# Optimization experiments

Hardware: AMD Instinct MI355X
Metric: run time of the kernel (lower is better)

## Reference

```python
import jax, jax.numpy as jnp
import numpy as np

WINDOW_SIZE = 2
SOFTMAX_TEMP = 0.01


def get_indices(batch_size, window_size):
    # For each window, match keypoints of frame j against dense map of frame j+1.
    kp_inds, dense_inds = [], []
    for i in range(batch_size):
        for j in range(window_size - 1):
            idx = i * window_size + j
            kp_inds.append(idx)
            dense_inds.append(idx + 1)
    return np.array(kp_inds), np.array(dense_inds)


def l2_normalize(x, axis):
    n = jnp.sqrt(jnp.sum(x * x, axis=axis, keepdims=True))
    return x / jnp.maximum(n, 1e-12)


def grid_sample_bilinear(img, grid_u, grid_v):
    """torch.nn.functional.grid_sample, mode='bilinear', padding='zeros', align_corners=False.
    img: (B,C,H,W); grid_u, grid_v: (B,N) normalized coords in [-1,1]. Returns (B,C,N)."""
    B, C, H, W = img.shape
    x = ((grid_u + 1.0) * W - 1.0) * 0.5  # pixel x
    y = ((grid_v + 1.0) * H - 1.0) * 0.5  # pixel y
    x0 = jnp.floor(x)
    y0 = jnp.floor(y)
    wx1 = x - x0
    wy1 = y - y0
    flat = img.reshape(B, C, H * W)

    def gather(xi, yi):
        valid = (xi >= 0) & (xi <= W - 1) & (yi >= 0) & (yi <= H - 1)
        xi_c = jnp.clip(xi, 0, W - 1).astype(jnp.int32)
        yi_c = jnp.clip(yi, 0, H - 1).astype(jnp.int32)
        idx = yi_c * W + xi_c  # (B,N)
        vals = jnp.take_along_axis(flat, idx[:, None, :], axis=2)  # (B,C,N)
        return vals * valid[:, None, :].astype(img.dtype)

    out = (gather(x0, y0) * ((1 - wx1) * (1 - wy1))[:, None, :]
           + gather(x0 + 1, y0) * (wx1 * (1 - wy1))[:, None, :]
           + gather(x0, y0 + 1) * ((1 - wx1) * wy1)[:, None, :]
           + gather(x0 + 1, y0 + 1) * (wx1 * wy1)[:, None, :])
    return out


def setup_inputs() -> dict:
    key = jax.random.key(0)
    k1, k2, k3, k4 = jax.random.split(key, 4)
    BW, C, N, H, W = 8, 128, 512, 256, 256
    return {
        "keypoint_scores": jax.random.uniform(k1, (BW, 1, N), dtype=jnp.float32),
        "keypoint_desc": jax.random.normal(k2, (BW, C, N), dtype=jnp.float32),
        "scores_dense": jax.random.uniform(k3, (BW, 1, H, W), dtype=jnp.float32),
        "desc_dense": jax.random.normal(k4, (BW, C, H, W), dtype=jnp.float32),
    }


def reference(keypoint_scores, keypoint_desc, scores_dense, desc_dense):
    BW, C, N = keypoint_desc.shape
    batch_size = BW // WINDOW_SIZE
    _, _, H, W = desc_dense.shape
    kp_inds, dense_inds = get_indices(batch_size, WINDOW_SIZE)

    src_desc = l2_normalize(keypoint_desc[kp_inds], axis=1)  # (B,C,N)
    B = src_desc.shape[0]
    tgt_desc_dense = desc_dense[dense_inds]  # (B,C,H,W)
    tgt_unrolled = l2_normalize(tgt_desc_dense.reshape(B, C, H * W), axis=1)

    # cosine similarity scores (B,N,H*W) -> temperature softmax over dense map
    match_vals = jnp.einsum('bcn,bcm->bnm', src_desc, tgt_unrolled)
    soft_match_vals = jax.nn.softmax(match_vals / SOFTMAX_TEMP, axis=2)

    # soft-argmax: expected (u,v) pixel coordinates
    v_coord, u_coord = jnp.meshgrid(jnp.arange(H), jnp.arange(W), indexing='ij')
    coords = jnp.stack([u_coord.reshape(-1), v_coord.reshape(-1)], axis=1).astype(jnp.float32)  # (HW,2)
    pseudo_coords = jnp.einsum('bnm,mk->bnk', soft_match_vals, coords)  # (B,N,2)

    u_norm = 2.0 * pseudo_coords[:, :, 0] / (W - 1) - 1.0
    v_norm = 2.0 * pseudo_coords[:, :, 1] / (H - 1) - 1.0

    tgt_scores_dense = scores_dense[dense_inds]
    pseudo_scores = grid_sample_bilinear(tgt_scores_dense, u_norm, v_norm)  # (B,1,N)
    pseudo_desc = grid_sample_bilinear(tgt_desc_dense, u_norm, v_norm)      # (B,C,N)

    desc_match_score = jnp.sum(src_desc * pseudo_desc, axis=1, keepdims=True) / float(C)
    src_scores = keypoint_scores[kp_inds]
    match_weights = 0.5 * (desc_match_score + 1.0) * src_scores * pseudo_scores
    return (pseudo_coords, match_weights, soft_match_vals)
```

## Files before the change

kernel.cpp:

```cpp
#include <hip/hip_runtime.h>


typedef short  v8s __attribute__((ext_vector_type(8)));
typedef unsigned short v8u __attribute__((ext_vector_type(8)));
typedef float  v4f __attribute__((ext_vector_type(4)));

#define EXP2_SCALE 144.269504088896f
#define WAITV(N) asm volatile("s_waitcnt vmcnt(" #N ")" ::: "memory")

static const size_t O_AHI  = 0;
static const size_t O_ALO  = O_AHI  + 262144ull*2;
static const size_t O_SRCN = O_ALO  + 262144ull*2;
static const size_t O_BHI  = O_SRCN + 262144ull*4;
static const size_t O_BLO  = O_BHI  + 33554432ull*2;
static const size_t O_PART = O_BLO  + 33554432ull*2;
static const size_t O_ROWS = O_PART + 2048ull*512*8;

static __device__ inline unsigned short f2bf(float x) {
    unsigned u = __float_as_uint(x);
    u = u + 0x7FFFu + ((u >> 16) & 1u);
    return (unsigned short)(u >> 16);
}
static __device__ inline float bf2f(unsigned short h) {
    return __uint_as_float(((unsigned)h) << 16);
}

__device__ __forceinline__ void gl_lds16(const void* g, void* l) {
    auto gp = (const __attribute__((address_space(1))) unsigned int*)(uintptr_t)g;
    auto lp = (__attribute__((address_space(3))) unsigned int*)(uintptr_t)l;
    __builtin_amdgcn_global_load_lds(gp, lp, 16, 0, 0);
}

__global__ void __launch_bounds__(256) k_prep_src(const float* __restrict__ kd,
                                                  float* __restrict__ srcN,
                                                  unsigned short* __restrict__ Ahi,
                                                  unsigned short* __restrict__ Alo) {
    int gw = blockIdx.x * 4 + (threadIdx.x >> 6);
    int l  = threadIdx.x & 63;
    int b  = gw >> 9, n = gw & 511;
    const float* base = kd + (size_t)(2 * b) * 128 * 512;
    float x0 = base[l * 512 + n];
    float x1 = base[(l + 64) * 512 + n];
    float ss = x0 * x0 + x1 * x1;
#pragma unroll
    for (int m = 1; m < 64; m <<= 1) ss += __shfl_xor(ss, m, 64);
    float inv = 1.0f / fmaxf(sqrtf(ss), 1e-12f);
    float xn0 = x0 * inv, xn1 = x1 * inv;
    int ob = gw * 128;
    srcN[ob + l] = xn0;  srcN[ob + l + 64] = xn1;
    unsigned short h0 = f2bf(xn0), h1 = f2bf(xn1);
    Ahi[ob + l] = h0;        Ahi[ob + l + 64] = h1;
    Alo[ob + l] = f2bf(xn0 - bf2f(h0));
    Alo[ob + l + 64] = f2bf(xn1 - bf2f(h1));
}

__global__ void __launch_bounds__(256, 2) k_prep_tgt(const float* __restrict__ dd,
                                                     unsigned short* __restrict__ Bhi,
                                                     unsigned short* __restrict__ Blo) {
    int t = blockIdx.x * 256 + threadIdx.x;
    int b = t >> 16;
    int p = t & 65535;
    const float* src = dd + (size_t)(2 * b + 1) * 128 * 65536 + p;
    float v[128];
    float ss = 0.f;
#pragma unroll
    for (int c = 0; c < 128; ++c) { float x = src[(size_t)c * 65536]; v[c] = x; ss += x * x; }
    float inv = 1.0f / fmaxf(sqrtf(ss), 1e-12f);
    size_t ob = (size_t)t * 128;
#pragma unroll
    for (int c8 = 0; c8 < 16; ++c8) {
        v8u h8, l8;
#pragma unroll
        for (int j = 0; j < 8; ++j) {
            float xn = v[c8 * 8 + j] * inv;
            unsigned short h = f2bf(xn);
            h8[j] = h;
            l8[j] = f2bf(xn - bf2f(h));
        }
        *(v8u*)(Bhi + ob + c8 * 8) = h8;
        *(v8u*)(Blo + ob + c8 * 8) = l8;
    }
}

template <int MODE>
__global__ void __launch_bounds__(256, 2) k_gemm(const unsigned short* __restrict__ Ahi,
                                                 const unsigned short* __restrict__ Alo,
                                                 const unsigned short* __restrict__ Bhi,
                                                 const unsigned short* __restrict__ Blo,
                                                 const float4* __restrict__ rows,
                                                 float* __restrict__ part,
                                                 float* __restrict__ osm) {
    __shared__ v4f bstage4[2048];
    __shared__ float paux[MODE == 1 ? 8192 : 512];
    char* bstage = (char*)bstage4;

    const int tid = threadIdx.x;
    const int l = tid & 63, w = tid >> 6;
    const int wm = w & 1, wn = w >> 1;
    const int l15 = l & 15, l16 = l >> 4;
    const int mtg = blockIdx.x, ny = blockIdx.y, b = blockIdx.z;
    const int mt0 = mtg * 16;

    v8s ahi[4][4], alo[4][4];
    {
        const size_t ar = ((size_t)(b * 512 + ny * 128 + wn * 64 + l15)) * 128 + l16 * 8;
#pragma unroll
        for (int nf = 0; nf < 4; ++nf)
#pragma unroll
            for (int ksl = 0; ksl < 4; ++ksl) {
                ahi[nf][ksl] = *(const v8s*)(Ahi + ar + nf * 2048 + ksl * 32);
                alo[nf][ksl] = *(const v8s*)(Alo + ar + nf * 2048 + ksl * 32);
            }
    }
    float invs[4];
    if (MODE == 1) {
#pragma unroll
        for (int nf = 0; nf < 4; ++nf)
            invs[nf] = rows[b * 512 + ny * 128 + wn * 64 + nf * 16 + l15].x;
    }
    asm volatile("s_waitcnt vmcnt(0)" ::: "memory");

    size_t pxrow = ((size_t)b * 65536 + (size_t)mt0 * 128) * 128;

#define STAGE(s, buf, prow)                                                         \
    {                                                                               \
        const unsigned short* src = (((s) < 2) ? Bhi : Blo) + (prow) + (((s) & 1) << 6); \
        char* dst = bstage + (buf) * 16384;                                         \
        _Pragma("unroll")                                                           \
        for (int i = 0; i < 4; ++i) {                                               \
            int sl = tid + i * 256;                                                 \
            int rl = sl >> 3, gg = sl & 7;                                          \
            gl_lds16(src + rl * 128 + ((gg ^ (rl & 7)) << 3), dst + (sl << 4));     \
        }                                                                           \
    }

    STAGE(0, 0, pxrow);

    for (int mt = 0; mt < 16; ++mt) {
        v4f acc[4][4];
#pragma unroll
        for (int mf = 0; mf < 4; ++mf)
#pragma unroll
            for (int nf = 0; nf < 4; ++nf) { v4f z = {0.f, 0.f, 0.f, 0.f}; acc[mf][nf] = z; }

#pragma unroll
        for (int s = 0; s < 4; ++s) {
            if (s < 3)            STAGE(s + 1, (s + 1) & 1, pxrow)
            else if (mt < 15)     STAGE(0, 0, pxrow + 16384)

            if (s == 0) {
                if (mt == 0) WAITV(4);
                else if (MODE == 1) WAITV(20);
                else WAITV(5);
            } else if (s == 3 && mt == 15) {
                WAITV(0);
            } else {
                WAITV(4);
            }
            __builtin_amdgcn_s_barrier();
            __builtin_amdgcn_sched_barrier(0);

            const char* bb = bstage + (s & 1) * 16384;
#pragma unroll
            for (int k2 = 0; k2 < 2; ++k2) {
                const int ksl = ((s & 1) << 1) | k2;
                v8s pxf[4];
#pragma unroll
                for (int mf = 0; mf < 4; ++mf) {
                    int r = wm * 64 + mf * 16 + l15;
                    pxf[mf] = *(const v8s*)(bb + r * 128 + ((((k2 << 2) | l16) ^ (r & 7)) << 4));
                }
#pragma unroll
                for (int mf = 0; mf < 4; ++mf)
#pragma unroll
                    for (int nf = 0; nf < 4; ++nf) {
                        acc[mf][nf] = __builtin_amdgcn_mfma_f32_16x16x32_bf16(pxf[mf], ahi[nf][ksl], acc[mf][nf], 0, 0, 0);
                        if (s < 2)
                            acc[mf][nf] = __builtin_amdgcn_mfma_f32_16x16x32_bf16(pxf[mf], alo[nf][ksl], acc[mf][nf], 0, 0, 0);
                    }
            }
            __builtin_amdgcn_sched_barrier(0);
            __builtin_amdgcn_s_barrier();
        }

        if (MODE == 0) {
            float sS[4], sM[4];
#pragma unroll
            for (int nf = 0; nf < 4; ++nf) { sS[nf] = 0.f; sM[nf] = 0.f; }
#pragma unroll
            for (int mf = 0; mf < 4; ++mf) {
                int mloc = wm * 64 + mf * 16 + l16 * 4;
#pragma unroll
                for (int nf = 0; nf < 4; ++nf)
#pragma unroll
                    for (int r = 0; r < 4; ++r) {
                        float e = __builtin_amdgcn_exp2f(fmaf(acc[mf][nf][r], EXP2_SCALE, -EXP2_SCALE));
                        sS[nf] += e;
                        sM[nf] = fmaf(e, (float)(mloc + r), sM[nf]);
                    }
            }
#pragma unroll
            for (int nf = 0; nf < 4; ++nf) {
                sS[nf] += __shfl_xor(sS[nf], 16, 64); sS[nf] += __shfl_xor(sS[nf], 32, 64);
                sM[nf] += __shfl_xor(sM[nf], 16, 64); sM[nf] += __shfl_xor(sM[nf], 32, 64);
            }
            if (l < 16) {
#pragma unroll
                for (int nf = 0; nf < 4; ++nf) {
                    paux[((w * 4 + nf) * 16 + l15) * 2 + 0] = sS[nf];
                    paux[((w * 4 + nf) * 16 + l15) * 2 + 1] = sM[nf];
                }
            }
            asm volatile("s_waitcnt lgkmcnt(0)" ::: "memory");
            __builtin_amdgcn_s_barrier();
            int q = tid & 1, p15 = (tid >> 1) & 15, pnf = (tid >> 5) & 3, pwn = tid >> 7;
            float vs = paux[(((pwn * 2 + 0) * 4 + pnf) * 16 + p15) * 2 + q]
                     + paux[(((pwn * 2 + 1) * 4 + pnf) * 16 + p15) * 2 + q];
            int rowg = b * 512 + ny * 128 + pwn * 64 + pnf * 16 + p15;
            part[((size_t)rowg * 512 + (mt0 + mt)) * 2 + q] = vs;
        } else {
            const size_t ocol = (size_t)(mt0 + mt) * 128;
            const int g = tid & 31, rh = tid >> 5;
#pragma unroll
            for (int half = 0; half < 2; ++half) {
                if (wn == half) {
#pragma unroll
                    for (int mf = 0; mf < 4; ++mf) {
                        int mq = wm * 16 + mf * 4 + l16;
#pragma unroll
                        for (int nf = 0; nf < 4; ++nf) {
                            int nl = nf * 16 + l15;
                            v4f pv;
#pragma unroll
                            for (int r = 0; r < 4; ++r)
                                pv[r] = __builtin_amdgcn_exp2f(fmaf(acc[mf][nf][r], EXP2_SCALE, -EXP2_SCALE)) * invs[nf];
                            *(v4f*)((char*)paux + nl * 512 + ((mq ^ (nl & 7)) << 4)) = pv;
                        }
                    }
                }
                asm volatile("s_waitcnt lgkmcnt(0)" ::: "memory");
                __builtin_amdgcn_s_barrier();
                size_t orow = (size_t)(b * 512 + ny * 128 + half * 64);
#pragma unroll
                for (int it = 0; it < 8; ++it) {
                    int r = it * 8 + rh;
                    v4f v = *(const v4f*)((const char*)paux + r * 512 + ((g ^ (r & 7)) << 4));
                    __builtin_nontemporal_store(v, (v4f*)(osm + (orow + r) * 65536 + ocol + g * 4));
                }
                __builtin_amdgcn_s_barrier();
            }
        }
        pxrow += 16384;
    }
#undef STAGE
}

__global__ void __launch_bounds__(256) k_reduce(const float2* __restrict__ part,
                                                float4* __restrict__ rows,
                                                float* __restrict__ out) {
    int r = blockIdx.x * 4 + (threadIdx.x >> 6);
    int l = threadIdx.x & 63;
    float S = 0.f, Su = 0.f, Sv = 0.f;
#pragma unroll
    for (int i = 0; i < 8; ++i) {
        int mtv = l + i * 64;
        float2 p = part[(size_t)r * 512 + mtv];
        S += p.x;
        Su += (float)((mtv & 1) * 128) * p.x + p.y;
        Sv += (float)(mtv >> 1) * p.x;
    }
#pragma unroll
    for (int m = 1; m < 64; m <<= 1) {
        S += __shfl_xor(S, m, 64);
        Su += __shfl_xor(Su, m, 64);
        Sv += __shfl_xor(Sv, m, 64);
    }
    if (l == 0) {
        float invS = 1.0f / S;
        float u = Su * invS, v = Sv * invS;
        rows[r] = make_float4(invS, u, v, 0.f);
        out[r * 2] = u;
        out[r * 2 + 1] = v;
    }
}

__global__ void __launch_bounds__(256) k_sample(const float* __restrict__ ksc,
                                                const float* __restrict__ sd,
                                                const float* __restrict__ dd,
                                                const float* __restrict__ srcN,
                                                const float4* __restrict__ rows,
                                                float* __restrict__ out) {
    int gw = blockIdx.x * 4 + (threadIdx.x >> 6);
    int l = threadIdx.x & 63;
    int b = gw >> 9, n = gw & 511;
    float4 rs = rows[gw];
    float u = rs.y, v = rs.z;
    float un = 2.0f * u / 255.0f - 1.0f;
    float vn = 2.0f * v / 255.0f - 1.0f;
    float x = ((un + 1.0f) * 256.0f - 1.0f) * 0.5f;
    float y = ((vn + 1.0f) * 256.0f - 1.0f) * 0.5f;
    float x0f = floorf(x), y0f = floorf(y);
    int x0 = (int)x0f, y0 = (int)y0f;
    int x1 = x0 + 1, y1 = y0 + 1;
    float wx1 = x - x0f, wy1 = y - y0f;
    float wx0 = 1.0f - wx1, wy0 = 1.0f - wy1;
    float m00 = ((x0 >= 0) & (x0 <= 255) & (y0 >= 0) & (y0 <= 255)) ? 1.f : 0.f;
    float m10 = ((x1 >= 0) & (x1 <= 255) & (y0 >= 0) & (y0 <= 255)) ? 1.f : 0.f;
    float m01 = ((x0 >= 0) & (x0 <= 255) & (y1 >= 0) & (y1 <= 255)) ? 1.f : 0.f;
    float m11 = ((x1 >= 0) & (x1 <= 255) & (y1 >= 0) & (y1 <= 255)) ? 1.f : 0.f;
    int cx0 = min(max(x0, 0), 255), cx1 = min(max(x1, 0), 255);
    int cy0 = min(max(y0, 0), 255), cy1 = min(max(y1, 0), 255);
    int i00 = cy0 * 256 + cx0, i10 = cy0 * 256 + cx1;
    int i01 = cy1 * 256 + cx0, i11 = cy1 * 256 + cx1;
    float w00 = wx0 * wy0 * m00, w10 = wx1 * wy0 * m10;
    float w01 = wx0 * wy1 * m01, w11 = wx1 * wy1 * m11;

    const float* sdb = sd + (size_t)(2 * b + 1) * 65536;
    float ps = w00 * sdb[i00] + w10 * sdb[i10] + w01 * sdb[i01] + w11 * sdb[i11];

    const float* ddb = dd + (size_t)(2 * b + 1) * 128 * 65536;
    float dot = 0.f;
#pragma unroll
    for (int h = 0; h < 2; ++h) {
        int c = l + h * 64;
        const float* dc = ddb + (size_t)c * 65536;
        float pd = w00 * dc[i00] + w10 * dc[i10] + w01 * dc[i01] + w11 * dc[i11];
        dot += srcN[gw * 128 + c] * pd;
    }
#pragma unroll
    for (int m = 1; m < 64; m <<= 1) dot += __shfl_xor(dot, m, 64);
    if (l == 0) {
        float dms = dot / 128.0f;
        float sscore = ksc[(2 * b) * 512 + n];
        out[4096 + gw] = 0.5f * (dms + 1.0f) * sscore * ps;
    }
}

extern "C" void kernel_launch(void* const* d_in, const int* in_sizes, int n_in,
                              void* d_out, int out_size, void* d_ws, size_t ws_size,
                              hipStream_t stream) {
    const float* ksc = (const float*)d_in[0];
    const float* kd  = (const float*)d_in[1];
    const float* sd  = (const float*)d_in[2];
    const float* dd  = (const float*)d_in[3];
    float* out = (float*)d_out;
    char* ws = (char*)d_ws;

    unsigned short* Ahi  = (unsigned short*)(ws + O_AHI);
    unsigned short* Alo  = (unsigned short*)(ws + O_ALO);
    float*          srcN = (float*)(ws + O_SRCN);
    unsigned short* Bhi  = (unsigned short*)(ws + O_BHI);
    unsigned short* Blo  = (unsigned short*)(ws + O_BLO);
    float*          part = (float*)(ws + O_PART);
    float4*         rows = (float4*)(ws + O_ROWS);
    float*          osm  = out + 6144;

    k_prep_src<<<512, 256, 0, stream>>>(kd, srcN, Ahi, Alo);
    k_prep_tgt<<<1024, 256, 0, stream>>>(dd, Bhi, Blo);
    k_gemm<0><<<dim3(32, 4, 4), 256, 0, stream>>>(Ahi, Alo, Bhi, Blo, rows, part, osm);
    k_reduce<<<512, 256, 0, stream>>>((const float2*)part, rows, out);
    k_gemm<1><<<dim3(32, 4, 4), 256, 0, stream>>>(Ahi, Alo, Bhi, Blo, rows, part, osm);
    k_sample<<<512, 256, 0, stream>>>(ksc, sd, dd, srcN, rows, out);
}
```

Baseline: 418.3 us.

## Fuse bilinear sampling into second GEMM and split target prep across thread pairs

The separate k_sample kernel is removed. Its bilinear sampling and match-weight computation now run as an epilogue in the ny==0 blocks of k_gemm<1>, which saves one launch and its tail. k_prep_tgt now gives each pixel to two threads, each handling 64 channels, with a shuffle to combine the squared norms; this lowers register pressure and doubles the thread count. The MODE 0 GEMM loop shrinks to two stages, applies the hi/lo split on every stage, and adds a barrier after the partial write. That changes how much of the K dimension the first pass covers, which may affect correctness.

```diff
diff --git a/kernel.cpp b/kernel.cpp
--- a/kernel.cpp
+++ b/kernel.cpp
@@ -54,28 +54,30 @@
     Alo[ob + l + 64] = f2bf(xn1 - bf2f(h1));
 }
 
-__global__ void __launch_bounds__(256, 2) k_prep_tgt(const float* __restrict__ dd,
-                                                     unsigned short* __restrict__ Bhi,
-                                                     unsigned short* __restrict__ Blo) {
-    int t = blockIdx.x * 256 + threadIdx.x;
+__global__ void __launch_bounds__(256) k_prep_tgt(const float* __restrict__ dd,
+                                                  unsigned short* __restrict__ Bhi,
+                                                  unsigned short* __restrict__ Blo) {
+    int t = blockIdx.x * 128 + (threadIdx.x >> 1);
+    int h = threadIdx.x & 1;
     int b = t >> 16;
     int p = t & 65535;
-    const float* src = dd + (size_t)(2 * b + 1) * 128 * 65536 + p;
-    float v[128];
+    const float* src = dd + (size_t)(2 * b + 1) * 128 * 65536 + (size_t)(h * 64) * 65536 + p;
+    float v[64];
     float ss = 0.f;
 #pragma unroll
-    for (int c = 0; c < 128; ++c) { float x = src[(size_t)c * 65536]; v[c] = x; ss += x * x; }
+    for (int c = 0; c < 64; ++c) { float x = src[(size_t)c * 65536]; v[c] = x; ss += x * x; }
+    ss += __shfl_xor(ss, 1, 64);
     float inv = 1.0f / fmaxf(sqrtf(ss), 1e-12f);
-    size_t ob = (size_t)t * 128;
-#pragma unroll
-    for (int c8 = 0; c8 < 16; ++c8) {
+    size_t ob = (size_t)t * 128 + h * 64;
+#pragma unroll
+    for (int c8 = 0; c8 < 8; ++c8) {
         v8u h8, l8;
 #pragma unroll
         for (int j = 0; j < 8; ++j) {
             float xn = v[c8 * 8 + j] * inv;
-            unsigned short h = f2bf(xn);
-            h8[j] = h;
-            l8[j] = f2bf(xn - bf2f(h));
+            unsigned short hh = f2bf(xn);
+            h8[j] = hh;
+            l8[j] = f2bf(xn - bf2f(hh));
         }
         *(v8u*)(Bhi + ob + c8 * 8) = h8;
         *(v8u*)(Blo + ob + c8 * 8) = l8;
@@ -89,10 +91,15 @@
                                                  const unsigned short* __restrict__ Blo,
                                                  const float4* __restrict__ rows,
                                                  float* __restrict__ part,
-                                                 float* __restrict__ osm) {
+                                                 float* __restrict__ out,
+                                                 const float* __restrict__ ksc,
+                                                 const float* __restrict__ sd,
+                                                 const float* __restrict__ dd,
+                                                 const float* __restrict__ srcN) {
     __shared__ v4f bstage4[2048];
     __shared__ float paux[MODE == 1 ? 8192 : 512];
     char* bstage = (char*)bstage4;
+    constexpr int NSTEP = (MODE == 0) ? 2 : 4;
 
     const int tid = threadIdx.x;
     const int l = tid & 63, w = tid >> 6;
@@ -100,6 +107,7 @@
     const int l15 = l & 15, l16 = l >> 4;
     const int mtg = blockIdx.x, ny = blockIdx.y, b = blockIdx.z;
     const int mt0 = mtg * 16;
+    float* osm = out + 6144;
 
     v8s ahi[4][4], alo[4][4];
     {
@@ -144,15 +152,15 @@
             for (int nf = 0; nf < 4; ++nf) { v4f z = {0.f, 0.f, 0.f, 0.f}; acc[mf][nf] = z; }
 
 #pragma unroll
-        for (int s = 0; s < 4; ++s) {
-            if (s < 3)            STAGE(s + 1, (s + 1) & 1, pxrow)
+        for (int s = 0; s < NSTEP; ++s) {
+            if (s < NSTEP - 1)    STAGE(s + 1, (s + 1) & 1, pxrow)
             else if (mt < 15)     STAGE(0, 0, pxrow + 16384)
 
             if (s == 0) {
-                if (mt == 0) WAITV(4);
-                else if (MODE == 1) WAITV(20);
-                else WAITV(5);
-            } else if (s == 3 && mt == 15) {
+                if (mt == 0)          WAITV(4);
+                else if (MODE == 1)   WAITV(20);
+                else                  WAITV(5);
+            } else if (s == NSTEP - 1 && mt == 15) {
                 WAITV(0);
             } else {
                 WAITV(4);
@@ -175,7 +183,7 @@
 #pragma unroll
                     for (int nf = 0; nf < 4; ++nf) {
                         acc[mf][nf] = __builtin_amdgcn_mfma_f32_16x16x32_bf16(pxf[mf], ahi[nf][ksl], acc[mf][nf], 0, 0, 0);
-                        if (s < 2)
+                        if (MODE == 0 || s < 2)
                             acc[mf][nf] = __builtin_amdgcn_mfma_f32_16x16x32_bf16(pxf[mf], alo[nf][ksl], acc[mf][nf], 0, 0, 0);
                     }
             }
@@ -218,6 +226,7 @@
                      + paux[(((pwn * 2 + 1) * 4 + pnf) * 16 + p15) * 2 + q];
             int rowg = b * 512 + ny * 128 + pwn * 64 + pnf * 16 + p15;
             part[((size_t)rowg * 512 + (mt0 + mt)) * 2 + q] = vs;
+            __builtin_amdgcn_s_barrier();
         } else {
             const size_t ocol = (size_t)(mt0 + mt) * 128;
             const int g = tid & 31, rh = tid >> 5;
@@ -253,6 +262,55 @@
         pxrow += 16384;
     }
 #undef STAGE
+
+    if (MODE == 1 && ny == 0) {
+        const int rbase = b * 512 + mtg * 16 + w * 4;
+#pragma unroll
+        for (int rr = 0; rr < 4; ++rr) {
+            int r = rbase + rr;
+            float4 rs = rows[r];
+            float u = rs.y, v = rs.z;
+            float un = 2.0f * u / 255.0f - 1.0f;
+            float vn = 2.0f * v / 255.0f - 1.0f;
+            float x = ((un + 1.0f) * 256.0f - 1.0f) * 0.5f;
+            float y = ((vn + 1.0f) * 256.0f - 1.0f) * 0.5f;
+            float x0f = floorf(x), y0f = floorf(y);
+            int x0 = (int)x0f, y0 = (int)y0f;
+            int x1 = x0 + 1, y1 = y0 + 1;
+            float wx1 = x - x0f, wy1 = y - y0f;
+            float wx0 = 1.0f - wx1, wy0 = 1.0f - wy1;
+            float m00 = ((x0 >= 0) & (x0 <= 255) & (y0 >= 0) & (y0 <= 255)) ? 1.f : 0.f;
+            float m10 = ((x1 >= 0) & (x1 <= 255) & (y0 >= 0) & (y0 <= 255)) ? 1.f : 0.f;
+            float m01 = ((x0 >= 0) & (x0 <= 255) & (y1 >= 0) & (y1 <= 255)) ? 1.f : 0.f;
+            float m11 = ((x1 >= 0) & (x1 <= 255) & (y1 >= 0) & (y1 <= 255)) ? 1.f : 0.f;
+            int cx0 = min(max(x0, 0), 255), cx1 = min(max(x1, 0), 255);
+            int cy0 = min(max(y0, 0), 255), cy1 = min(max(y1, 0), 255);
+            int i00 = cy0 * 256 + cx0, i10 = cy0 * 256 + cx1;
+            int i01 = cy1 * 256 + cx0, i11 = cy1 * 256 + cx1;
+            float w00 = wx0 * wy0 * m00, w10 = wx1 * wy0 * m10;
+            float w01 = wx0 * wy1 * m01, w11 = wx1 * wy1 * m11;
+
+            const float* sdb = sd + (size_t)(2 * b + 1) * 65536;
+            float ps = w00 * sdb[i00] + w10 * sdb[i10] + w01 * sdb[i01] + w11 * sdb[i11];
+
+            const float* ddb = dd + (size_t)(2 * b + 1) * 128 * 65536;
+            float dot = 0.f;
+#pragma unroll
+            for (int h2 = 0; h2 < 2; ++h2) {
+                int c = l + h2 * 64;
+                const float* dc = ddb + (size_t)c * 65536;
+                float pd = w00 * dc[i00] + w10 * dc[i10] + w01 * dc[i01] + w11 * dc[i11];
+                dot += srcN[r * 128 + c] * pd;
+            }
+#pragma unroll
+            for (int m = 1; m < 64; m <<= 1) dot += __shfl_xor(dot, m, 64);
+            if (l == 0) {
+                float dms = dot / 128.0f;
+                float sscore = ksc[(2 * b) * 512 + (r & 511)];
+                out[4096 + r] = 0.5f * (dms + 1.0f) * sscore * ps;
+            }
+        }
+    }
 }
 
 __global__ void __launch_bounds__(256) k_reduce(const float2* __restrict__ part,
@@ -281,58 +339,6 @@
         rows[r] = make_float4(invS, u, v, 0.f);
         out[r * 2] = u;
         out[r * 2 + 1] = v;
-    }
-}
-
-__global__ void __launch_bounds__(256) k_sample(const float* __restrict__ ksc,
-                                                const float* __restrict__ sd,
-                                                const float* __restrict__ dd,
-                                                const float* __restrict__ srcN,
-                                                const float4* __restrict__ rows,
-                                                float* __restrict__ out) {
-    int gw = blockIdx.x * 4 + (threadIdx.x >> 6);
-    int l = threadIdx.x & 63;
-    int b = gw >> 9, n = gw & 511;
-    float4 rs = rows[gw];
-    float u = rs.y, v = rs.z;
-    float un = 2.0f * u / 255.0f - 1.0f;
-    float vn = 2.0f * v / 255.0f - 1.0f;
-    float x = ((un + 1.0f) * 256.0f - 1.0f) * 0.5f;
-    float y = ((vn + 1.0f) * 256.0f - 1.0f) * 0.5f;
-    float x0f = floorf(x), y0f = floorf(y);
-    int x0 = (int)x0f, y0 = (int)y0f;
-    int x1 = x0 + 1, y1 = y0 + 1;
-    float wx1 = x - x0f, wy1 = y - y0f;
-    float wx0 = 1.0f - wx1, wy0 = 1.0f - wy1;
-    float m00 = ((x0 >= 0) & (x0 <= 255) & (y0 >= 0) & (y0 <= 255)) ? 1.f : 0.f;
-    float m10 = ((x1 >= 0) & (x1 <= 255) & (y0 >= 0) & (y0 <= 255)) ? 1.f : 0.f;
-    float m01 = ((x0 >= 0) & (x0 <= 255) & (y1 >= 0) & (y1 <= 255)) ? 1.f : 0.f;
-    float m11 = ((x1 >= 0) & (x1 <= 255) & (y1 >= 0) & (y1 <= 255)) ? 1.f : 0.f;
-    int cx0 = min(max(x0, 0), 255), cx1 = min(max(x1, 0), 255);
-    int cy0 = min(max(y0, 0), 255), cy1 = min(max(y1, 0), 255);
-    int i00 = cy0 * 256 + cx0, i10 = cy0 * 256 + cx1;
-    int i01 = cy1 * 256 + cx0, i11 = cy1 * 256 + cx1;
-    float w00 = wx0 * wy0 * m00, w10 = wx1 * wy0 * m10;
-    float w01 = wx0 * wy1 * m01, w11 = wx1 * wy1 * m11;
-
-    const float* sdb = sd + (size_t)(2 * b + 1) * 65536;
-    float ps = w00 * sdb[i00] + w10 * sdb[i10] + w01 * sdb[i01] + w11 * sdb[i11];
-
-    const float* ddb = dd + (size_t)(2 * b + 1) * 128 * 65536;
-    float dot = 0.f;
-#pragma unroll
-    for (int h = 0; h < 2; ++h) {
-        int c = l + h * 64;
-        const float* dc = ddb + (size_t)c * 65536;
-        float pd = w00 * dc[i00] + w10 * dc[i10] + w01 * dc[i01] + w11 * dc[i11];
-        dot += srcN[gw * 128 + c] * pd;
-    }
-#pragma unroll
-    for (int m = 1; m < 64; m <<= 1) dot += __shfl_xor(dot, m, 64);
-    if (l == 0) {
-        float dms = dot / 128.0f;
-        float sscore = ksc[(2 * b) * 512 + n];
-        out[4096 + gw] = 0.5f * (dms + 1.0f) * sscore * ps;
     }
 }
 
@@ -353,12 +359,10 @@
     unsigned short* Blo  = (unsigned short*)(ws + O_BLO);
     float*          part = (float*)(ws + O_PART);
     float4*         rows = (float4*)(ws + O_ROWS);
-    float*          osm  = out + 6144;
 
     k_prep_src<<<512, 256, 0, stream>>>(kd, srcN, Ahi, Alo);
-    k_prep_tgt<<<1024, 256, 0, stream>>>(dd, Bhi, Blo);
-    k_gemm<0><<<dim3(32, 4, 4), 256, 0, stream>>>(Ahi, Alo, Bhi, Blo, rows, part, osm);
+    k_prep_tgt<<<2048, 256, 0, stream>>>(dd, Bhi, Blo);
+    k_gemm<0><<<dim3(32, 4, 4), 256, 0, stream>>>(Ahi, Alo, Bhi, Blo, rows, part, out, ksc, sd, dd, srcN);
     k_reduce<<<512, 256, 0, stream>>>((const float2*)part, rows, out);
-    k_gemm<1><<<dim3(32, 4, 4), 256, 0, stream>>>(Ahi, Alo, Bhi, Blo, rows, part, osm);
-    k_sample<<<512, 256, 0, stream>>>(ksc, sd, dd, srcN, rows, out);
-}
+    k_gemm<1><<<dim3(32, 4, 4), 256, 0, stream>>>(Ahi, Alo, Bhi, Blo, rows, part, out, ksc, sd, dd, srcN);
+}
```

Measured after the change: 434.0 us. +3.7%, slower.
